# Performance work log

Hardware: AMD Instinct MI355X
Metric: run time of the kernel (lower is better)

Reference implementation:

```python
import jax, jax.numpy as jnp
import numpy as np

NEG_SLOPE = 0.2


def _gat_conv(x, edge_index, W, a_src, a_dst, b, heads, out_ch, concat):
    N = x.shape[0]
    # add self loops (PyG GATConv default)
    loops = jnp.arange(N, dtype=edge_index.dtype)
    src = jnp.concatenate([edge_index[0], loops])
    dst = jnp.concatenate([edge_index[1], loops])

    h = (x @ W).reshape(N, heads, out_ch)            # [N,H,C]
    alpha_s = jnp.einsum('nhc,hc->nh', h, a_src)     # [N,H]
    alpha_d = jnp.einsum('nhc,hc->nh', h, a_dst)     # [N,H]
    e = jax.nn.leaky_relu(alpha_s[src] + alpha_d[dst], NEG_SLOPE)  # [E,H]

    # softmax over incoming edges of each dst node (every node has a self loop)
    m = jax.ops.segment_max(e, dst, num_segments=N)  # [N,H]
    e = jnp.exp(e - m[dst])
    denom = jax.ops.segment_sum(e, dst, num_segments=N)  # [N,H]
    alpha = e / denom[dst]                           # [E,H]

    out = jax.ops.segment_sum(h[src] * alpha[..., None], dst, num_segments=N)  # [N,H,C]
    out = out.reshape(N, heads * out_ch) if concat else out.mean(axis=1)
    return out + b


def setup_inputs() -> dict:
    key = jax.random.key(0)
    ks = jax.random.split(key, 12)
    N, E = 100000, 3200000
    F_IN, HID, H1, H2, NCLS = 7, 8, 8, 1, 2
    x = jax.random.normal(ks[0], (N, F_IN), dtype=jnp.float32)
    edge_index = jax.random.randint(ks[1], (2, E), 0, N, dtype=jnp.int64)
    s1 = 1.0 / np.sqrt(F_IN)
    s2 = 1.0 / np.sqrt(HID * H1)
    return {
        'x': x,
        'edge_index': edge_index,
        'W1': jax.random.uniform(ks[2], (F_IN, H1 * HID), jnp.float32, -s1, s1),
        'a_src1': jax.random.uniform(ks[3], (H1, HID), jnp.float32, -s1, s1),
        'a_dst1': jax.random.uniform(ks[4], (H1, HID), jnp.float32, -s1, s1),
        'b1': jnp.zeros((H1 * HID,), jnp.float32),
        'W2': jax.random.uniform(ks[5], (H1 * HID, H2 * NCLS), jnp.float32, -s2, s2),
        'a_src2': jax.random.uniform(ks[6], (H2, NCLS), jnp.float32, -s2, s2),
        'a_dst2': jax.random.uniform(ks[7], (H2, NCLS), jnp.float32, -s2, s2),
        'b2': jnp.zeros((NCLS,), jnp.float32),
    }


def reference(x, edge_index, W1, a_src1, a_dst1, b1, W2, a_src2, a_dst2, b2):
    # eval mode: dropout is identity
    h = _gat_conv(x, edge_index, W1, a_src1, a_dst1, b1, heads=8, out_ch=8, concat=True)
    h = jax.nn.elu(h)
    out = _gat_conv(h, edge_index, W2, a_src2, a_dst2, b2, heads=1, out_ch=2, concat=False)
    return jax.nn.log_softmax(out, axis=1)
```

## Files before the change

kernel.cpp:

```cpp
#include <hip/hip_runtime.h>
#include <math.h>

#define NEG_SLOPE 0.2f
#define L2E 1.4426950408889634f
#define NPB_SHIFT 8
#define NBMAX 512
#define SC_EDGES 16384
#define SC_THREADS 1024
#define CAP 9216
#define CAPN 96

typedef unsigned int u32x4 __attribute__((ext_vector_type(4)));
typedef int i32x4 __attribute__((ext_vector_type(4)));

__device__ __forceinline__ unsigned short f2bf(float f) {
    unsigned int u = __float_as_uint(f);
    u += 0x7FFFu + ((u >> 16) & 1u);
    return (unsigned short)(u >> 16);
}

__global__ void k_h1_scatter(const float* __restrict__ x, const float* __restrict__ W1,
                             const float* __restrict__ a_dst,
                             int N, char* __restrict__ rec,
                             float* __restrict__ ad1,
                             const int* __restrict__ srcA, const int* __restrict__ dstA,
                             int E, int sb, int* __restrict__ cursor_g,
                             unsigned int* __restrict__ payload) {
    __shared__ union {
        struct { int hist[NBMAX]; int gbase[NBMAX]; } sc;
        float ws[7 * 64];
    } smem;
    int t = threadIdx.x;

    if ((int)blockIdx.x < sb) {
        const int ITER = SC_EDGES / SC_THREADS;
        unsigned pay[ITER];
        int meta[ITER];
        int base = blockIdx.x * SC_EDGES;
        int cnt = E - base; if (cnt > SC_EDGES) cnt = SC_EDGES;
        for (int i = t; i < NBMAX; i += SC_THREADS) smem.sc.hist[i] = 0;
        __syncthreads();
#define PROC(ki, dv, sv) {                                                    \
            int bb = (dv) >> NPB_SHIFT;                                       \
            pay[ki] = ((unsigned int)((dv) & ((1 << NPB_SHIFT) - 1)) << 24)   \
                      | (unsigned int)(sv);                                   \
            int r = atomicAdd(&smem.sc.hist[bb], 1);                          \
            meta[ki] = (bb << 15) | r; }
#pragma unroll
        for (int k = 0; k < ITER / 4; ++k) {
            int j = (k * SC_THREADS + t) * 4;
            if (j + 3 < cnt) {
                i32x4 d4 = __builtin_nontemporal_load((const i32x4*)(dstA + base + j));
                i32x4 s4 = __builtin_nontemporal_load((const i32x4*)(srcA + base + j));
                PROC(4 * k + 0, d4[0], s4[0]);
                PROC(4 * k + 1, d4[1], s4[1]);
                PROC(4 * k + 2, d4[2], s4[2]);
                PROC(4 * k + 3, d4[3], s4[3]);
            } else {
#pragma unroll
                for (int u = 0; u < 4; ++u) {
                    int j2 = j + u;
                    if (j2 < cnt) {
                        int d = __builtin_nontemporal_load(dstA + base + j2);
                        int s = __builtin_nontemporal_load(srcA + base + j2);
                        PROC(4 * k + u, d, s);
                    } else {
                        meta[4 * k + u] = -1;
                    }
                }
            }
        }
#undef PROC
        __syncthreads();
        for (int b = t; b < NBMAX; b += SC_THREADS) {
            int c = smem.sc.hist[b];
            smem.sc.gbase[b] = c ? atomicAdd(&cursor_g[b], c) : 0;
        }
        __syncthreads();
#pragma unroll
        for (int k = 0; k < ITER; ++k) {
            if (meta[k] >= 0) {
                int b = meta[k] >> 15;
                int r = meta[k] & 0x7FFF;
                int pos = smem.sc.gbase[b] + r;
                if ((unsigned)pos < CAP)
                    payload[(size_t)b * CAP + pos] = pay[k];
            }
        }
        return;
    }

    for (int i = t; i < 7 * 64; i += SC_THREADS) smem.ws[i] = W1[i];
    __syncthreads();
    int lane = t & 63;
    int base_n = (blockIdx.x - sb) * 64 + (t >> 6) * 4;
    float adv = a_dst[lane];
#pragma unroll
    for (int u = 0; u < 4; ++u) {
        int n = base_n + u;
        if (n >= N) break;
        float hv = 0.f;
#pragma unroll
        for (int k = 0; k < 7; ++k) hv += x[n * 7 + k] * smem.ws[k * 64 + lane];
        ((unsigned short*)(rec + ((size_t)n << 7)))[lane] = f2bf(hv);
        float pd = hv * adv;
#pragma unroll
        for (int off = 1; off < 8; off <<= 1) pd += __shfl_xor(pd, off);
        if ((lane & 7) == 0) ad1[n * 8 + (lane >> 3)] = pd * L2E;
    }
}

__global__ void k_buildcsr(const unsigned int* __restrict__ payload,
                           const int* __restrict__ cursor_g, int N,
                           int2* __restrict__ nrow, int* __restrict__ csr) {
    __shared__ int hist[256];
    int b = blockIdx.x;
    int t = threadIdx.x;
    int cntb = cursor_g[b]; if (cntb > CAP) cntb = CAP;
    int bs = b * CAP;
    int nodeBase = b << NPB_SHIFT;
    int nNodes = N - nodeBase; if (nNodes > 256) nNodes = 256;
    if (t < 256) hist[t] = 0;
    __syncthreads();
#define PUT(w) {                                                       \
        int dl = (int)((w) >> 24);                                     \
        int r = atomicAdd(&hist[dl], 1);                               \
        if (r < CAPN)                                                  \
            csr[(size_t)(nodeBase + dl) * CAPN + r] = (int)((w) & 0xFFFFFFu); }
#pragma unroll
    for (int k = 0; k < (CAP + 4095) / 4096; ++k) {
        int j = (k * 1024 + t) * 4;
        if (j + 3 < cntb) {
            u32x4 p4 = __builtin_nontemporal_load((const u32x4*)(payload + bs + j));
            PUT(p4[0]); PUT(p4[1]); PUT(p4[2]); PUT(p4[3]);
        } else {
            for (int u = 0; u < 4; ++u) {
                int j2 = j + u;
                if (j2 < cntb) {
                    unsigned w = __builtin_nontemporal_load(payload + bs + j2);
                    PUT(w);
                }
            }
        }
    }
#undef PUT
    __syncthreads();
    if (t < nNodes)
        nrow[nodeBase + t] = make_int2(min(hist[t], CAPN), (nodeBase + t) * CAPN);
}

__device__ __forceinline__ void oct_core(
    u32x4 f, float4 awA, float4 awB, float adv, float wm,
    float& den, float& a0, float& a1, float& a2, float& a3,
    float& a4, float& a5, float& a6, float& a7) {
    float f0 = __uint_as_float(f[0] << 16);
    float f1 = __uint_as_float(f[0] & 0xFFFF0000u);
    float f2 = __uint_as_float(f[1] << 16);
    float f3 = __uint_as_float(f[1] & 0xFFFF0000u);
    float f4 = __uint_as_float(f[2] << 16);
    float f5 = __uint_as_float(f[2] & 0xFFFF0000u);
    float f6 = __uint_as_float(f[3] << 16);
    float f7 = __uint_as_float(f[3] & 0xFFFF0000u);
    float p = fmaf(f0, awA.x, adv);
    float q = f1 * awA.y;
    p = fmaf(f2, awA.z, p);
    q = fmaf(f3, awA.w, q);
    p = fmaf(f4, awB.x, p);
    q = fmaf(f5, awB.y, q);
    p = fmaf(f6, awB.z, p);
    q = fmaf(f7, awB.w, q);
    float t = p + q;
    float w = __builtin_amdgcn_exp2f(fmaxf(t, NEG_SLOPE * t)) * wm;
    den += w;
    a0 = fmaf(w, f0, a0);
    a1 = fmaf(w, f1, a1);
    a2 = fmaf(w, f2, a2);
    a3 = fmaf(w, f3, a3);
    a4 = fmaf(w, f4, a4);
    a5 = fmaf(w, f5, a5);
    a6 = fmaf(w, f6, a6);
    a7 = fmaf(w, f7, a7);
}

__global__ void k_agg1(const char* __restrict__ rec, const float* __restrict__ asW,
                       const float* __restrict__ ad1,
                       const int2* __restrict__ nrow,
                       const int* __restrict__ csr, const float* __restrict__ b1,
                       const float* __restrict__ W2, const float* __restrict__ as2w,
                       const float* __restrict__ ad2w, int N,
                       float4* __restrict__ pack) {
    int lane = threadIdx.x & 63;
    int qtr  = lane >> 4;
    int n0 = blockIdx.x * 16 + (threadIdx.x >> 6) * 4 + qtr;
    int n = n0 < N ? n0 : N - 1;
    int ql = lane & 7;
    int s  = (lane >> 3) & 1;
    unsigned foff = (unsigned)(ql << 4);
    float4 awA = ((const float4*)asW)[2 * ql];
    float4 awB = ((const float4*)asW)[2 * ql + 1];
    awA.x *= L2E; awA.y *= L2E; awA.z *= L2E; awA.w *= L2E;
    awB.x *= L2E; awB.y *= L2E; awB.z *= L2E; awB.w *= L2E;
    float adv = ad1[n * 8 + ql];
    int2 dr = nrow[n];
    int d = dr.x;
    int start = dr.y;
    const int* csrb = csr + start;
    int dm1 = d - 1;
    int dmx = max(d, __shfl_xor(d, 16));
    dmx = max(dmx, __shfl_xor(dmx, 32));
    int dmx_s = __builtin_amdgcn_readfirstlane(dmx);
    float a0 = 0.f, a1 = 0.f, a2 = 0.f, a3 = 0.f;
    float a4 = 0.f, a5 = 0.f, a6 = 0.f, a7 = 0.f;
    float den = 0.f;
#define LDR(sv) (*(const u32x4*)(rec + (size_t)((((unsigned)(sv)) << 7) + foff)))
#define QIDX(p) max(min((p), dm1), 0)
    int i1a = csrb[QIDX(s)];
    int i1b = csrb[QIDX(s + 2)];
    int i2a = csrb[QIDX(s + 4)];
    int i2b = csrb[QIDX(s + 6)];
    u32x4 g0a = LDR(i1a);
    u32x4 g0b = LDR(i1b);
    int nst = (dmx_s + 3) >> 2;
#pragma unroll 2
    for (int st = 0; st < nst; ++st) {
        int base4 = st * 4;
        int i3a = csrb[QIDX(base4 + 8 + s)];
        int i3b = csrb[QIDX(base4 + 10 + s)];
        u32x4 g1a = LDR(i2a);
        u32x4 g1b = LDR(i2b);
        float wma = (base4 + s     < d) ? 1.f : 0.f;
        float wmb = (base4 + s + 2 < d) ? 1.f : 0.f;
        oct_core(g0a, awA, awB, adv, wma, den, a0, a1, a2, a3, a4, a5, a6, a7);
        oct_core(g0b, awA, awB, adv, wmb, den, a0, a1, a2, a3, a4, a5, a6, a7);
        g0a = g1a; g0b = g1b;
        i2a = i3a; i2b = i3b;
        (void)i1a; (void)i1b;
    }
    {
        float wm = (s == 0) ? 1.f : 0.f;
        oct_core(LDR(n), awA, awB, adv, wm,
                 den, a0, a1, a2, a3, a4, a5, a6, a7);
    }
#undef QIDX
#undef LDR
    den += __shfl_xor(den, 8);
    a0 += __shfl_xor(a0, 8);
    a1 += __shfl_xor(a1, 8);
    a2 += __shfl_xor(a2, 8);
    a3 += __shfl_xor(a3, 8);
    a4 += __shfl_xor(a4, 8);
    a5 += __shfl_xor(a5, 8);
    a6 += __shfl_xor(a6, 8);
    a7 += __shfl_xor(a7, 8);
    float rden = 1.f / den;
    float4 bbA = ((const float4*)b1)[2 * ql];
    float4 bbB = ((const float4*)b1)[2 * ql + 1];
    float o0 = a0 * rden + bbA.x;
    float o1 = a1 * rden + bbA.y;
    float o2 = a2 * rden + bbA.z;
    float o3 = a3 * rden + bbA.w;
    float o4 = a4 * rden + bbB.x;
    float o5 = a5 * rden + bbB.y;
    float o6 = a6 * rden + bbB.z;
    float o7 = a7 * rden + bbB.w;
    float v0 = o0 > 0.f ? o0 : (__expf(o0) - 1.f);
    float v1 = o1 > 0.f ? o1 : (__expf(o1) - 1.f);
    float v2 = o2 > 0.f ? o2 : (__expf(o2) - 1.f);
    float v3 = o3 > 0.f ? o3 : (__expf(o3) - 1.f);
    float v4 = o4 > 0.f ? o4 : (__expf(o4) - 1.f);
    float v5 = o5 > 0.f ? o5 : (__expf(o5) - 1.f);
    float v6 = o6 > 0.f ? o6 : (__expf(o6) - 1.f);
    float v7 = o7 > 0.f ? o7 : (__expf(o7) - 1.f);
    const float4* W2v = (const float4*)W2;
    float4 w20 = W2v[4 * ql + 0];
    float4 w21 = W2v[4 * ql + 1];
    float4 w22 = W2v[4 * ql + 2];
    float4 w23 = W2v[4 * ql + 3];
    float p0 = v0 * w20.x + v1 * w20.z + v2 * w21.x + v3 * w21.z
             + v4 * w22.x + v5 * w22.z + v6 * w23.x + v7 * w23.z;
    float p1 = v0 * w20.y + v1 * w20.w + v2 * w21.y + v3 * w21.w
             + v4 * w22.y + v5 * w22.w + v6 * w23.y + v7 * w23.w;
#pragma unroll
    for (int off = 1; off < 8; off <<= 1) {
        p0 += __shfl_xor(p0, off);
        p1 += __shfl_xor(p1, off);
    }
    if ((lane & 15) == 0 && n0 < N) {
        float4 pk;
        pk.x = p0;
        pk.y = p1;
        pk.z = (p0 * as2w[0] + p1 * as2w[1]) * L2E;
        pk.w = (p0 * ad2w[0] + p1 * ad2w[1]) * L2E;
        pack[n] = pk;
    }
}

__global__ void k_agg2(const float4* __restrict__ pack, const int2* __restrict__ nrow,
                       const int* __restrict__ csr,
                       const float* __restrict__ b2, int N, float* __restrict__ out) {
    int n = blockIdx.x * 16 + (threadIdx.x >> 4);
    int hl = threadIdx.x & 15;
    if (n >= N) return;
    float4 self = pack[n];
    float adv = self.w;
    int2 dr = nrow[n];
    int d = dr.x;
    int start = dr.y;
    float den = 0.f, a0 = 0.f, a1 = 0.f;
    for (int i = hl; i < d; i += 16) {
        int src = __builtin_nontemporal_load(csr + start + i);
        float4 q = pack[src];
        float t = q.z + adv;
        float w = __builtin_amdgcn_exp2f(fmaxf(t, NEG_SLOPE * t));
        den += w;
        a0 += w * q.x;
        a1 += w * q.y;
    }
#pragma unroll
    for (int off = 1; off < 16; off <<= 1) {
        den += __shfl_xor(den, off);
        a0  += __shfl_xor(a0, off);
        a1  += __shfl_xor(a1, off);
    }
    if (hl == 0) {
        float t = self.z + adv;
        float w = __builtin_amdgcn_exp2f(fmaxf(t, NEG_SLOPE * t));
        den += w;
        a0 += w * self.x;
        a1 += w * self.y;
        float o0 = a0 / den + b2[0];
        float o1 = a1 / den + b2[1];
        float m = fmaxf(o0, o1);
        float lse = m + logf(__expf(o0 - m) + __expf(o1 - m));
        out[n * 2 + 0] = o0 - lse;
        out[n * 2 + 1] = o1 - lse;
    }
}

extern "C" void kernel_launch(void* const* d_in, const int* in_sizes, int n_in,
                              void* d_out, int out_size, void* d_ws, size_t ws_size,
                              hipStream_t stream) {
    const float* x     = (const float*)d_in[0];
    const int*   ei    = (const int*)d_in[1];
    const float* W1    = (const float*)d_in[2];
    const float* as1w  = (const float*)d_in[3];
    const float* ad1w  = (const float*)d_in[4];
    const float* b1    = (const float*)d_in[5];
    const float* W2    = (const float*)d_in[6];
    const float* as2w  = (const float*)d_in[7];
    const float* ad2w  = (const float*)d_in[8];
    const float* b2    = (const float*)d_in[9];
    float* out = (float*)d_out;

    const int N = in_sizes[0] / 7;
    const int E = in_sizes[1] / 2;
    const int* srcA = ei;
    const int* dstA = ei + E;
    const int NB = (N + ((1 << NPB_SHIFT) - 1)) >> NPB_SHIFT;

    size_t off = 0;
    auto alloc = [&](size_t bytes) -> void* {
        void* p = (char*)d_ws + off;
        off += (bytes + 255) & ~(size_t)255;
        return p;
    };
    unsigned int* payload = (unsigned int*)alloc((size_t)NB * CAP * 4);
    char*  rec  = (char*)alloc((size_t)N * 128);
    float* ad1  = (float*)alloc((size_t)N * 8 * 4);
    float4* pack = (float4*)alloc((size_t)N * 16);
    int2*  nrow = (int2*)alloc((size_t)N * 8);
    int*   csr  = (int*)alloc((size_t)NB * 256 * CAPN * 4);
    int*   cursor_g = (int*)alloc(NBMAX * 4);

    const int nb2 = (N + 63) / 64;
    const int sb  = (E + SC_EDGES - 1) / SC_EDGES;
    const int nb  = (N + 15) / 16;

    hipMemsetAsync(cursor_g, 0, NBMAX * 4, stream);
    k_h1_scatter<<<sb + nb2, SC_THREADS, 0, stream>>>(x, W1, ad1w, N, rec, ad1,
                                                      srcA, dstA, E, sb, cursor_g, payload);
    k_buildcsr<<<NB, 1024, 0, stream>>>(payload, cursor_g, N, nrow, csr);
    k_agg1<<<nb, 256, 0, stream>>>(rec, as1w, ad1, nrow, csr, b1,
                                   W2, as2w, ad2w, N, pack);
    k_agg2<<<(N + 15) / 16, 256, 0, stream>>>(pack, nrow, csr, b2, N, out);
}
```

Before: 209.2 us.

## Sort nodes by degree within each bucket to balance agg1 wavefronts

The CSR build kernel now counts node degrees per 256-node bucket, prefix-scans them and writes a permutation that orders each bucket's nodes by in-degree. k_agg1 reads nodes through this permutation, so the four nodes sharing a wavefront have similar degrees and the loop bound (the max degree across the wave) wastes fewer iterations. The cost is extra scan and sync work in buildcsr, an extra indirection, and less contiguous access to ad1/nrow/pack. Padded slots map to node N-1, which gets recomputed and written redundantly.

```diff
diff --git a/kernel.cpp b/kernel.cpp
--- a/kernel.cpp
+++ b/kernel.cpp
@@ -112,8 +112,10 @@
 
 __global__ void k_buildcsr(const unsigned int* __restrict__ payload,
                            const int* __restrict__ cursor_g, int N,
-                           int2* __restrict__ nrow, int* __restrict__ csr) {
+                           int2* __restrict__ nrow, int* __restrict__ csr,
+                           int* __restrict__ perm) {
     __shared__ int hist[256];
+    __shared__ int dcnt[128], dscan[128], dctr[128];
     int b = blockIdx.x;
     int t = threadIdx.x;
     int cntb = cursor_g[b]; if (cntb > CAP) cntb = CAP;
@@ -121,6 +123,7 @@
     int nodeBase = b << NPB_SHIFT;
     int nNodes = N - nodeBase; if (nNodes > 256) nNodes = 256;
     if (t < 256) hist[t] = 0;
+    if (t >= 256 && t < 384) { dcnt[t - 256] = 0; dctr[t - 256] = 0; }
     __syncthreads();
 #define PUT(w) {                                                       \
         int dl = (int)((w) >> 24);                                     \
@@ -145,8 +148,29 @@
     }
 #undef PUT
     __syncthreads();
-    if (t < nNodes)
-        nrow[nodeBase + t] = make_int2(min(hist[t], CAPN), (nodeBase + t) * CAPN);
+    int dg = -1;
+    if (t < nNodes) {
+        dg = min(hist[t], CAPN);
+        nrow[nodeBase + t] = make_int2(dg, (nodeBase + t) * CAPN);
+        atomicAdd(&dcnt[dg], 1);
+    }
+    __syncthreads();
+    if (t < 128) dscan[t] = dcnt[t];
+    __syncthreads();
+    for (int off = 1; off < 128; off <<= 1) {
+        int u = 0;
+        if (t < 128 && t >= off) u = dscan[t - off];
+        __syncthreads();
+        if (t < 128) dscan[t] += u;
+        __syncthreads();
+    }
+    if (t < nNodes) {
+        int r = atomicAdd(&dctr[dg], 1);
+        int pos = dscan[dg] - dcnt[dg] + r;
+        perm[nodeBase + pos] = nodeBase + t;
+    } else if (t < 256) {
+        perm[nodeBase + t] = N - 1;
+    }
 }
 
 __device__ __forceinline__ void oct_core(
@@ -188,11 +212,12 @@
                        const int* __restrict__ csr, const float* __restrict__ b1,
                        const float* __restrict__ W2, const float* __restrict__ as2w,
                        const float* __restrict__ ad2w, int N,
+                       const int* __restrict__ perm,
                        float4* __restrict__ pack) {
     int lane = threadIdx.x & 63;
     int qtr  = lane >> 4;
-    int n0 = blockIdx.x * 16 + (threadIdx.x >> 6) * 4 + qtr;
-    int n = n0 < N ? n0 : N - 1;
+    int idx  = (blockIdx.x & 15) * 16 + (threadIdx.x >> 6) * 4 + qtr;
+    int n = perm[((blockIdx.x >> 4) << 8) + idx];
     int ql = lane & 7;
     int s  = (lane >> 3) & 1;
     unsigned foff = (unsigned)(ql << 4);
@@ -285,7 +310,7 @@
         p0 += __shfl_xor(p0, off);
         p1 += __shfl_xor(p1, off);
     }
-    if ((lane & 15) == 0 && n0 < N) {
+    if ((lane & 15) == 0) {
         float4 pk;
         pk.x = p0;
         pk.y = p1;
@@ -370,17 +395,18 @@
     float4* pack = (float4*)alloc((size_t)N * 16);
     int2*  nrow = (int2*)alloc((size_t)N * 8);
     int*   csr  = (int*)alloc((size_t)NB * 256 * CAPN * 4);
+    int*   perm = (int*)alloc((size_t)NB * 256 * 4);
     int*   cursor_g = (int*)alloc(NBMAX * 4);
 
     const int nb2 = (N + 63) / 64;
     const int sb  = (E + SC_EDGES - 1) / SC_EDGES;
-    const int nb  = (N + 15) / 16;
+    const int nb1 = NB * 16;
 
     hipMemsetAsync(cursor_g, 0, NBMAX * 4, stream);
     k_h1_scatter<<<sb + nb2, SC_THREADS, 0, stream>>>(x, W1, ad1w, N, rec, ad1,
                                                       srcA, dstA, E, sb, cursor_g, payload);
-    k_buildcsr<<<NB, 1024, 0, stream>>>(payload, cursor_g, N, nrow, csr);
-    k_agg1<<<nb, 256, 0, stream>>>(rec, as1w, ad1, nrow, csr, b1,
-                                   W2, as2w, ad2w, N, pack);
+    k_buildcsr<<<NB, 1024, 0, stream>>>(payload, cursor_g, N, nrow, csr, perm);
+    k_agg1<<<nb1, 256, 0, stream>>>(rec, as1w, ad1, nrow, csr, b1,
+                                    W2, as2w, ad2w, N, perm, pack);
     k_agg2<<<(N + 15) / 16, 256, 0, stream>>>(pack, nrow, csr, b2, N, out);
 }
```

Result: slower. 218.5 us (+4.4%).
